# Kernel tuning notes

Hardware: AMD Instinct MI355X
Metric: run time of the kernel (lower is better)

## Reference

```python
import jax, jax.numpy as jnp
import numpy as np

EMBED = 256
HEADS = 8
WH, WW = 7, 7
N = WH * WW


def _rel_pos_index(Wh, Ww):
    coords = np.stack(np.meshgrid(np.arange(Wh), np.arange(Ww), indexing='ij'))  # [2,Wh,Ww]
    flat = coords.reshape(2, -1)  # [2, N]
    rel = flat[:, :, None] - flat[:, None, :]  # [2,N,N]
    rel = rel.transpose(1, 2, 0).astype(np.int64)
    rel[:, :, 0] += Wh - 1
    rel[:, :, 1] += Ww - 1
    rel[:, :, 0] *= 2 * Ww - 1
    return rel.sum(-1)  # [N,N]


def setup_inputs() -> dict:
    key = jax.random.key(0)
    ks = jax.random.split(key, 8)
    B = 4096
    nW = 64
    x = jax.random.normal(ks[0], (B, N, EMBED), dtype=jnp.float32)
    mask = jax.random.normal(ks[1], (nW, N, N), dtype=jnp.float32)
    qkv_w = jax.random.normal(ks[2], (3 * EMBED, EMBED), dtype=jnp.float32) * (EMBED ** -0.5)
    qkv_b = jnp.zeros((3 * EMBED,), dtype=jnp.float32)
    proj_w = jax.random.normal(ks[3], (EMBED, EMBED), dtype=jnp.float32) * (EMBED ** -0.5)
    proj_b = jnp.zeros((EMBED,), dtype=jnp.float32)
    bias_table = jax.random.normal(ks[4], ((2 * WH - 1) * (2 * WW - 1), HEADS), dtype=jnp.float32) * 0.02
    return {"x": x, "mask": mask, "qkv_w": qkv_w, "qkv_b": qkv_b,
            "proj_w": proj_w, "proj_b": proj_b, "bias_table": bias_table}


def reference(x, mask, qkv_w, qkv_b, proj_w, proj_b, bias_table):
    B, n, C = x.shape
    hd = C // HEADS
    scale = hd ** -0.5
    rel_idx = jnp.asarray(_rel_pos_index(WH, WW))  # [N,N] int, static
    qkv = (x @ qkv_w.T + qkv_b).reshape(B, n, 3, HEADS, hd)
    qkv = jnp.transpose(qkv, (2, 0, 3, 1, 4))  # [3,B,H,N,hd]
    q, k, v = qkv[0] * scale, qkv[1], qkv[2]
    attn = jnp.einsum('bhqd,bhkd->bhqk', q, k)  # [B,H,N,N]
    rel_bias = bias_table[rel_idx]  # [N,N,H]
    attn = attn + jnp.transpose(rel_bias, (2, 0, 1))[None]
    nW = mask.shape[0]
    attn = attn.reshape(B // nW, nW, HEADS, n, n) + mask[None, :, None]
    attn = attn.reshape(B, HEADS, n, n)
    attn = jax.nn.softmax(attn, axis=-1)
    out = jnp.einsum('bhqk,bhkd->bhqd', attn, v)  # [B,H,N,hd]
    out = jnp.transpose(out, (0, 2, 1, 3)).reshape(B, n, C)
    return out @ proj_w.T + proj_b
```

## Files before the change

### kernel.cpp

```cpp
#include <hip/hip_runtime.h>
#include <hip/hip_bf16.h>

typedef __bf16 bf16x8 __attribute__((ext_vector_type(8)));
typedef float f32x4 __attribute__((ext_vector_type(4)));
typedef short short8 __attribute__((ext_vector_type(8)));
typedef short short4v __attribute__((ext_vector_type(4)));

#define XSTRIDE 264
#define SCRSZ   2560
#define QKSTR   20
#define QHALF   1280
#define VSTR    72
#define PSTR    72
#define PBUF    1152

#define WS_QW   256u
#define WS_PW   393472u
#define WS_QB   524544u
#define WS_PB   527616u
#define WS_CMB  528640u
#define WS_FULL (528640u + 8388608u)

__device__ __forceinline__ float b2f(short s) {
  unsigned u = ((unsigned)(unsigned short)s) << 16;
  float f; __builtin_memcpy(&f, &u, 4); return f;
}
__device__ __forceinline__ short f2b(float f) {
  unsigned u; __builtin_memcpy(&u, &f, 4);
  u += 0x7FFFu + ((u >> 16) & 1u);
  return (short)(u >> 16);
}
__device__ __forceinline__ bf16x8 ld8(const short* p) {
  short8 s = *(const short8*)p;
  bf16x8 f; __builtin_memcpy(&f, &s, 16); return f;
}
__device__ __forceinline__ float ldE(const void* p, size_t i, int f32) {
  return f32 ? ((const float*)p)[i] : b2f(((const short*)p)[i]);
}
__device__ __forceinline__ f32x4 mfma16(bf16x8 a, bf16x8 b, f32x4 c) {
  return __builtin_amdgcn_mfma_f32_16x16x32_bf16(a, b, c, 0, 0, 0);
}
__device__ __forceinline__ void lgkm0() {
  asm volatile("s_waitcnt lgkmcnt(0)" ::: "memory");
  __builtin_amdgcn_sched_barrier(0);
}

__global__ __launch_bounds__(256) void detect_k(
    const short* p0, int n0, const short* p1, int n1, const short* p2, int n2,
    const short* p3, int n3, const short* p4, int n4, const short* p5, int n5,
    const short* p6, int n6, int* flags)
{
  const short* ps[7] = {p0, p1, p2, p3, p4, p5, p6};
  int ns[7] = {n0, n1, n2, n3, n4, n5, n6};
  int b = blockIdx.x;
  const short* p = ps[b];
  int n = ns[b];
  __shared__ int mx;
  if (threadIdx.x == 0) mx = 0;
  __syncthreads();
  int K = n >> 1; if (K > 4096) K = 4096;
  int lm = 0;
  for (int k = threadIdx.x; k < K; k += 256) {
    int e = (((int)(unsigned short)p[2 * k]) >> 7) & 0xFF;
    lm = lm > e ? lm : e;
  }
  atomicMax(&mx, lm);
  __syncthreads();
  if (threadIdx.x == 0) flags[b] = (mx >= 160) ? 1 : 0;
}

__global__ __launch_bounds__(256) void prep_k(
    const void* __restrict__ qkvw, const void* __restrict__ qkvb,
    const void* __restrict__ projw, const void* __restrict__ projb,
    const void* __restrict__ btab, const void* __restrict__ maskg,
    char* __restrict__ ws, const int* __restrict__ flags, int use_cmb)
{
  const int fm = flags[1], fqw = flags[2], fqb = flags[3];
  const int fpw = flags[4], fpb = flags[5], fbt = flags[6];
  short* qw = (short*)(ws + WS_QW);
  short* pw = (short*)(ws + WS_PW);
  float* qb = (float*)(ws + WS_QB);
  float* pb = (float*)(ws + WS_PB);
  float* cmb = (float*)(ws + WS_CMB);
  const int blk = blockIdx.x, tid = threadIdx.x;
  if (blk < 512) {
    if (!use_cmb) return;
    int widx = blk >> 3, h = blk & 7;
    for (int i = tid; i < 4096; i += 256) {
      int tq = i >> 6, tk = i & 63;
      float v = -1e30f;
      if (tq < 49 && tk < 49) {
        int qr = tq / 7, qc = tq - qr * 7;
        int kr = tk / 7, kc = tk - kr * 7;
        int idx = (qr - kr + 6) * 13 + (qc - kc + 6);
        v = ldE(maskg, (size_t)widx * 2401 + tq * 49 + tk, fm)
          + ldE(btab, (size_t)idx * 8 + h, fbt);
      }
      cmb[(size_t)blk * 4096 + i] = v;
    }
  } else if (blk < 528) {
    int base = (blk - 512) * 12288;
    for (int i = tid; i < 12288; i += 256)
      qw[base + i] = f2b(ldE(qkvw, base + i, fqw));
  } else if (blk < 530) {
    int base = (blk - 528) * 32768;
    for (int i = tid; i < 32768; i += 256)
      pw[base + i] = f2b(ldE(projw, base + i, fpw));
  } else {
    for (int i = tid; i < 768; i += 256) qb[i] = ldE(qkvb, i, fqb);
    if (tid < 256) pb[tid] = ldE(projb, tid, fpb);
  }
}

template<int USE_CMB>
__global__ __launch_bounds__(512, 4) void wmsa(
    const void* __restrict__ xg, const void* __restrict__ maskg,
    const void* __restrict__ btab, const char* __restrict__ ws,
    void* __restrict__ outg, const int* __restrict__ flags)
{
  __shared__ __align__(16) short lds[37376];
  const int tid  = threadIdx.x;
  const int w    = tid >> 6;
  const int lane = tid & 63;
  const int L    = lane & 15;
  const int quad = lane >> 4;
  const int b    = blockIdx.x;

  const int fx = flags[0];
  const int fm = flags[1], fbt = flags[6];

  const short* qw  = (const short*)(ws + WS_QW);
  const short* pw  = (const short*)(ws + WS_PW);
  const float* qb  = (const float*)(ws + WS_QB);
  const float* pb  = (const float*)(ws + WS_PB);
  const float* cmb = (const float*)(ws + WS_CMB);

  short* x_s = lds;
  short* scr = lds + 16896 + w * SCRSZ;

  if (fx) {
    const float* xb = (const float*)xg + (size_t)b * (49 * 256);
    for (int i = tid; i < 1568; i += 512) {
      int t = i >> 5, c8 = i & 31;
      const float* s = xb + t * 256 + c8 * 8;
      f32x4 a = *(const f32x4*)s;
      f32x4 c = *(const f32x4*)(s + 4);
      short8 v;
      v[0] = f2b(a[0]); v[1] = f2b(a[1]); v[2] = f2b(a[2]); v[3] = f2b(a[3]);
      v[4] = f2b(c[0]); v[5] = f2b(c[1]); v[6] = f2b(c[2]); v[7] = f2b(c[3]);
      *(short8*)(x_s + t * XSTRIDE + c8 * 8) = v;
    }
  } else {
    const short* xb = (const short*)xg + (size_t)b * (49 * 256);
    for (int i = tid; i < 1568; i += 512) {
      int t = i >> 5, c8 = i & 31;
      *(short8*)(x_s + t * XSTRIDE + c8 * 8) = *(const short8*)(xb + t * 256 + c8 * 8);
    }
  }
  for (int i = tid; i < 495; i += 512) {
    int t = 49 + i / 33, c8 = i - (i / 33) * 33;
    *(short8*)(x_s + t * XSTRIDE + c8 * 8) = short8{0,0,0,0,0,0,0,0};
  }
  __syncthreads();

  const int h = w;
  const float scale = 0.17677669529663687f;
  bf16x8 fq[4], fk[4], fv[2][2];

  {
    const int baserow = h * 32;
    bf16x8 wf[16];
    #pragma unroll
    for (int nbo = 0; nbo < 2; nbo++) {
      const short* wr = qw + (size_t)(baserow + nbo * 16 + L) * 256 + quad * 8;
      #pragma unroll
      for (int ks = 0; ks < 8; ks++) wf[nbo * 8 + ks] = ld8(wr + ks * 32);
    }
    const float b0 = qb[baserow + L], b1 = qb[baserow + 16 + L];
    #pragma unroll
    for (int m = 0; m < 4; m++) {
      const short* ar = x_s + (m * 16 + L) * XSTRIDE + quad * 8;
      bf16x8 xf[8];
      #pragma unroll
      for (int ks = 0; ks < 8; ks++) xf[ks] = ld8(ar + ks * 32);
      f32x4 a0 = {0.f,0.f,0.f,0.f}, a1 = {0.f,0.f,0.f,0.f};
      #pragma unroll
      for (int ks = 0; ks < 8; ks++) {
        a0 = mfma16(xf[ks], wf[ks], a0);
        a1 = mfma16(xf[ks], wf[8 + ks], a1);
      }
      #pragma unroll
      for (int r = 0; r < 4; r++) {
        scr[(m * 16 + quad * 4 + r) * QKSTR + L]         = f2b((a0[r] + b0) * scale);
        scr[QHALF + (m * 16 + quad * 4 + r) * QKSTR + L] = f2b((a1[r] + b1) * scale);
      }
    }
  }
  lgkm0();
  #pragma unroll
  for (int nbq = 0; nbq < 4; nbq++)
    fq[nbq] = ld8(scr + (quad >> 1) * QHALF + (nbq * 16 + L) * QKSTR + (quad & 1) * 8);
  lgkm0();

  {
    const int baserow = 256 + h * 32;
    bf16x8 wf[16];
    #pragma unroll
    for (int nbo = 0; nbo < 2; nbo++) {
      const short* wr = qw + (size_t)(baserow + nbo * 16 + L) * 256 + quad * 8;
      #pragma unroll
      for (int ks = 0; ks < 8; ks++) wf[nbo * 8 + ks] = ld8(wr + ks * 32);
    }
    const float b0 = qb[baserow + L], b1 = qb[baserow + 16 + L];
    #pragma unroll
    for (int m = 0; m < 4; m++) {
      const short* ar = x_s + (m * 16 + L) * XSTRIDE + quad * 8;
      bf16x8 xf[8];
      #pragma unroll
      for (int ks = 0; ks < 8; ks++) xf[ks] = ld8(ar + ks * 32);
      f32x4 a0 = {0.f,0.f,0.f,0.f}, a1 = {0.f,0.f,0.f,0.f};
      #pragma unroll
      for (int ks = 0; ks < 8; ks++) {
        a0 = mfma16(xf[ks], wf[ks], a0);
        a1 = mfma16(xf[ks], wf[8 + ks], a1);
      }
      #pragma unroll
      for (int r = 0; r < 4; r++) {
        scr[(m * 16 + quad * 4 + r) * QKSTR + L]         = f2b(a0[r] + b0);
        scr[QHALF + (m * 16 + quad * 4 + r) * QKSTR + L] = f2b(a1[r] + b1);
      }
    }
  }
  lgkm0();
  #pragma unroll
  for (int m = 0; m < 4; m++)
    fk[m] = ld8(scr + (quad >> 1) * QHALF + (m * 16 + L) * QKSTR + (quad & 1) * 8);
  lgkm0();

  #pragma unroll
  for (int nbo = 0; nbo < 2; nbo++) {
    const int baserow = 512 + h * 32 + nbo * 16;
    const short* wr = qw + (size_t)(baserow + L) * 256 + quad * 8;
    bf16x8 wf[8];
    #pragma unroll
    for (int ks = 0; ks < 8; ks++) wf[ks] = ld8(wr + ks * 32);
    const float bias = qb[baserow + L];
    #pragma unroll
    for (int m = 0; m < 4; m++) {
      const short* ar = x_s + (m * 16 + L) * XSTRIDE + quad * 8;
      f32x4 acc = {0.f, 0.f, 0.f, 0.f};
      #pragma unroll
      for (int ks = 0; ks < 8; ks++) acc = mfma16(ld8(ar + ks * 32), wf[ks], acc);
      short4v pk;
      #pragma unroll
      for (int r = 0; r < 4; r++) pk[r] = f2b(acc[r] + bias);
      *(short4v*)(scr + (nbo * 16 + L) * VSTR + m * 16 + quad * 4) = pk;
    }
  }
  lgkm0();
  #pragma unroll
  for (int ks2 = 0; ks2 < 2; ks2++)
    #pragma unroll
    for (int blk2 = 0; blk2 < 2; blk2++)
      fv[ks2][blk2] = ld8(scr + (blk2 * 16 + L) * VSTR + ks2 * 32 + quad * 8);
  lgkm0();

  __syncthreads();

  const int widx = b & 63;
  const float* cmbh = cmb + ((size_t)(widx * 8 + h)) * 4096;
  short* o_s = lds;
  #pragma unroll
  for (int nbq = 0; nbq < 4; nbq++) {
    const int tq = nbq * 16 + L;
    f32x4 c4[4];
    if (USE_CMB) {
      #pragma unroll
      for (int m = 0; m < 4; m++)
        c4[m] = *(const f32x4*)(cmbh + tq * 64 + m * 16 + quad * 4);
    }
    f32x4 s[4];
    #pragma unroll
    for (int m = 0; m < 4; m++) {
      f32x4 z = {0.f, 0.f, 0.f, 0.f};
      s[m] = mfma16(fk[m], fq[nbq], z);
    }
    float vals[16];
    float mx = -1e30f;
    if (USE_CMB) {
      #pragma unroll
      for (int m = 0; m < 4; m++) {
        #pragma unroll
        for (int r = 0; r < 4; r++) {
          float v = s[m][r] + c4[m][r];
          vals[m * 4 + r] = v;
          mx = fmaxf(mx, v);
        }
      }
    } else {
      const int tqc = tq < 49 ? tq : 48;
      const int qr = tqc / 7, qc = tqc - qr * 7;
      #pragma unroll
      for (int m = 0; m < 4; m++) {
        #pragma unroll
        for (int r = 0; r < 4; r++) {
          const int tk = m * 16 + quad * 4 + r;
          float v = -1e30f;
          if (tk < 49) {
            const int kr = tk / 7, kc = tk - kr * 7;
            const int idx = (qr - kr + 6) * 13 + (qc - kc + 6);
            v = s[m][r] + ldE(btab, (size_t)idx * 8 + h, fbt)
                        + ldE(maskg, (size_t)widx * 2401 + tqc * 49 + tk, fm);
          }
          vals[m * 4 + r] = v;
          mx = fmaxf(mx, v);
        }
      }
    }
    mx = fmaxf(mx, __shfl_xor(mx, 16));
    mx = fmaxf(mx, __shfl_xor(mx, 32));
    float sum = 0.f;
    #pragma unroll
    for (int i2 = 0; i2 < 16; i2++) { vals[i2] = __expf(vals[i2] - mx); sum += vals[i2]; }
    sum += __shfl_xor(sum, 16);
    sum += __shfl_xor(sum, 32);
    const float inv = 1.f / sum;
    short* pbuf = scr + (nbq & 1) * PBUF;
    #pragma unroll
    for (int m = 0; m < 4; m++) {
      short4v pk;
      #pragma unroll
      for (int r = 0; r < 4; r++) pk[r] = f2b(vals[m * 4 + r] * inv);
      *(short4v*)(pbuf + L * PSTR + m * 16 + quad * 4) = pk;
    }
    lgkm0();
    f32x4 o0 = {0.f,0.f,0.f,0.f}, o1 = {0.f,0.f,0.f,0.f};
    #pragma unroll
    for (int ks2 = 0; ks2 < 2; ks2++) {
      bf16x8 fp = ld8(pbuf + L * PSTR + ks2 * 32 + quad * 8);
      o0 = mfma16(fp, fv[ks2][0], o0);
      o1 = mfma16(fp, fv[ks2][1], o1);
    }
    #pragma unroll
    for (int r = 0; r < 4; r++) {
      o_s[(nbq * 16 + quad * 4 + r) * XSTRIDE + h * 32 + L]      = f2b(o0[r]);
      o_s[(nbq * 16 + quad * 4 + r) * XSTRIDE + h * 32 + 16 + L] = f2b(o1[r]);
    }
  }
  __syncthreads();

  {
    const int mb = w & 3, half = w >> 2;
    bf16x8 ao[8];
    const short* orow = o_s + (mb * 16 + L) * XSTRIDE + quad * 8;
    #pragma unroll
    for (int ks = 0; ks < 8; ks++) ao[ks] = ld8(orow + ks * 32);
    int nb = half * 8;
    bf16x8 cur[8];
    {
      const short* wr = pw + (size_t)(nb * 16 + L) * 256 + quad * 8;
      #pragma unroll
      for (int ks = 0; ks < 8; ks++) cur[ks] = ld8(wr + ks * 32);
    }
    for (int i = 0; i < 8; i++, nb++) {
      bf16x8 nxt[8];
      if (i < 7) {
        const short* wr = pw + (size_t)((nb + 1) * 16 + L) * 256 + quad * 8;
        #pragma unroll
        for (int ks = 0; ks < 8; ks++) nxt[ks] = ld8(wr + ks * 32);
      }
      f32x4 acc = {0.f, 0.f, 0.f, 0.f};
      #pragma unroll
      for (int ks = 0; ks < 8; ks++) acc = mfma16(ao[ks], cur[ks], acc);
      const float bias = pb[nb * 16 + L];
      #pragma unroll
      for (int r = 0; r < 4; r++) {
        const int t = mb * 16 + quad * 4 + r;
        if (t < 49) {
          size_t ofs = (size_t)b * (49 * 256) + (size_t)t * 256 + nb * 16 + L;
          float val = acc[r] + bias;
          if (fx) ((float*)outg)[ofs] = val;
          else    ((short*)outg)[ofs] = f2b(val);
        }
      }
      #pragma unroll
      for (int ks = 0; ks < 8; ks++) cur[ks] = nxt[ks];
    }
  }
}

extern "C" void kernel_launch(void* const* d_in, const int* in_sizes, int n_in,
                              void* d_out, int out_size, void* d_ws, size_t ws_size,
                              hipStream_t stream) {
  (void)n_in; (void)out_size;
  int B = in_sizes[0] / (49 * 256);
  char* ws = (char*)d_ws;
  int* flags = (int*)ws;
  detect_k<<<7, 256, 0, stream>>>(
      (const short*)d_in[0], in_sizes[0], (const short*)d_in[1], in_sizes[1],
      (const short*)d_in[2], in_sizes[2], (const short*)d_in[3], in_sizes[3],
      (const short*)d_in[4], in_sizes[4], (const short*)d_in[5], in_sizes[5],
      (const short*)d_in[6], in_sizes[6], flags);
  const int use_cmb = ws_size >= (size_t)WS_FULL;
  prep_k<<<531, 256, 0, stream>>>(d_in[2], d_in[3], d_in[4], d_in[5], d_in[6],
                                  d_in[1], ws, flags, use_cmb);
  if (use_cmb)
    wmsa<1><<<B, 512, 0, stream>>>(d_in[0], d_in[1], d_in[6], ws, d_out, flags);
  else
    wmsa<0><<<B, 512, 0, stream>>>(d_in[0], d_in[1], d_in[6], ws, d_out, flags);
}
```

Before: 824.2 us.

## Prefetch weights and mask tiles earlier, transpose MFMA operands for vectorized LDS stores

Q weight fragments are now loaded from global memory before the x tile is staged into LDS, and the first projection weight tile is loaded before the barrier, so global latency overlaps other work. Mask/bias tiles are double-buffered across query blocks instead of being loaded just before use. The MFMA operands for Q/K and PV are swapped so each lane's results land along one row, which allows 4-wide short stores to a single packed scratch layout and removes the explicit lgkmcnt waits and scheduling barriers. The trade-off is more live registers (wfQ held across staging, c4p double buffer), which may pressure occupancy at 512 threads and 4 blocks per CU.

Measured after the change: 827.8 us. No clear change (+0.4%).

```diff
diff --git a/kernel.cpp b/kernel.cpp
--- a/kernel.cpp
+++ b/kernel.cpp
@@ -7,9 +7,8 @@
 typedef short short4v __attribute__((ext_vector_type(4)));
 
 #define XSTRIDE 264
-#define SCRSZ   2560
-#define QKSTR   20
-#define QHALF   1280
+#define SCRSZ   2304
+#define QKSTR   36
 #define VSTR    72
 #define PSTR    72
 #define PBUF    1152
@@ -39,10 +38,6 @@
 }
 __device__ __forceinline__ f32x4 mfma16(bf16x8 a, bf16x8 b, f32x4 c) {
   return __builtin_amdgcn_mfma_f32_16x16x32_bf16(a, b, c, 0, 0, 0);
-}
-__device__ __forceinline__ void lgkm0() {
-  asm volatile("s_waitcnt lgkmcnt(0)" ::: "memory");
-  __builtin_amdgcn_sched_barrier(0);
 }
 
 __global__ __launch_bounds__(256) void detect_k(
@@ -118,7 +113,7 @@
     const void* __restrict__ btab, const char* __restrict__ ws,
     void* __restrict__ outg, const int* __restrict__ flags)
 {
-  __shared__ __align__(16) short lds[37376];
+  __shared__ __align__(16) short lds[35328];
   const int tid  = threadIdx.x;
   const int w    = tid >> 6;
   const int lane = tid & 63;
@@ -137,6 +132,18 @@
 
   short* x_s = lds;
   short* scr = lds + 16896 + w * SCRSZ;
+
+  const int h = w;
+
+  bf16x8 wfQ[16];
+  {
+    #pragma unroll
+    for (int cht = 0; cht < 2; cht++) {
+      const short* wr = qw + (size_t)(h * 32 + cht * 16 + L) * 256 + quad * 8;
+      #pragma unroll
+      for (int ks = 0; ks < 8; ks++) wfQ[cht * 8 + ks] = ld8(wr + ks * 32);
+    }
+  }
 
   if (fx) {
     const float* xb = (const float*)xg + (size_t)b * (49 * 256);
@@ -163,20 +170,12 @@
   }
   __syncthreads();
 
-  const int h = w;
   const float scale = 0.17677669529663687f;
   bf16x8 fq[4], fk[4], fv[2][2];
 
   {
-    const int baserow = h * 32;
-    bf16x8 wf[16];
-    #pragma unroll
-    for (int nbo = 0; nbo < 2; nbo++) {
-      const short* wr = qw + (size_t)(baserow + nbo * 16 + L) * 256 + quad * 8;
-      #pragma unroll
-      for (int ks = 0; ks < 8; ks++) wf[nbo * 8 + ks] = ld8(wr + ks * 32);
-    }
-    const float b0 = qb[baserow + L], b1 = qb[baserow + 16 + L];
+    const f32x4 b4a = *(const f32x4*)(qb + h * 32 + quad * 4);
+    const f32x4 b4b = *(const f32x4*)(qb + h * 32 + 16 + quad * 4);
     #pragma unroll
     for (int m = 0; m < 4; m++) {
       const short* ar = x_s + (m * 16 + L) * XSTRIDE + quad * 8;
@@ -186,32 +185,33 @@
       f32x4 a0 = {0.f,0.f,0.f,0.f}, a1 = {0.f,0.f,0.f,0.f};
       #pragma unroll
       for (int ks = 0; ks < 8; ks++) {
-        a0 = mfma16(xf[ks], wf[ks], a0);
-        a1 = mfma16(xf[ks], wf[8 + ks], a1);
-      }
+        a0 = mfma16(wfQ[ks], xf[ks], a0);
+        a1 = mfma16(wfQ[8 + ks], xf[ks], a1);
+      }
+      short4v q0, q1;
       #pragma unroll
       for (int r = 0; r < 4; r++) {
-        scr[(m * 16 + quad * 4 + r) * QKSTR + L]         = f2b((a0[r] + b0) * scale);
-        scr[QHALF + (m * 16 + quad * 4 + r) * QKSTR + L] = f2b((a1[r] + b1) * scale);
-      }
-    }
-  }
-  lgkm0();
+        q0[r] = f2b((a0[r] + b4a[r]) * scale);
+        q1[r] = f2b((a1[r] + b4b[r]) * scale);
+      }
+      *(short4v*)(scr + (m * 16 + L) * QKSTR + quad * 4)      = q0;
+      *(short4v*)(scr + (m * 16 + L) * QKSTR + 16 + quad * 4) = q1;
+    }
+  }
   #pragma unroll
   for (int nbq = 0; nbq < 4; nbq++)
-    fq[nbq] = ld8(scr + (quad >> 1) * QHALF + (nbq * 16 + L) * QKSTR + (quad & 1) * 8);
-  lgkm0();
-
-  {
-    const int baserow = 256 + h * 32;
-    bf16x8 wf[16];
-    #pragma unroll
-    for (int nbo = 0; nbo < 2; nbo++) {
-      const short* wr = qw + (size_t)(baserow + nbo * 16 + L) * 256 + quad * 8;
-      #pragma unroll
-      for (int ks = 0; ks < 8; ks++) wf[nbo * 8 + ks] = ld8(wr + ks * 32);
-    }
-    const float b0 = qb[baserow + L], b1 = qb[baserow + 16 + L];
+    fq[nbq] = ld8(scr + (nbq * 16 + L) * QKSTR + quad * 8);
+
+  {
+    bf16x8 wfK[16];
+    #pragma unroll
+    for (int cht = 0; cht < 2; cht++) {
+      const short* wr = qw + (size_t)(256 + h * 32 + cht * 16 + L) * 256 + quad * 8;
+      #pragma unroll
+      for (int ks = 0; ks < 8; ks++) wfK[cht * 8 + ks] = ld8(wr + ks * 32);
+    }
+    const f32x4 b4a = *(const f32x4*)(qb + 256 + h * 32 + quad * 4);
+    const f32x4 b4b = *(const f32x4*)(qb + 256 + h * 32 + 16 + quad * 4);
     #pragma unroll
     for (int m = 0; m < 4; m++) {
       const short* ar = x_s + (m * 16 + L) * XSTRIDE + quad * 8;
@@ -221,64 +221,77 @@
       f32x4 a0 = {0.f,0.f,0.f,0.f}, a1 = {0.f,0.f,0.f,0.f};
       #pragma unroll
       for (int ks = 0; ks < 8; ks++) {
-        a0 = mfma16(xf[ks], wf[ks], a0);
-        a1 = mfma16(xf[ks], wf[8 + ks], a1);
-      }
+        a0 = mfma16(wfK[ks], xf[ks], a0);
+        a1 = mfma16(wfK[8 + ks], xf[ks], a1);
+      }
+      short4v k0, k1;
       #pragma unroll
       for (int r = 0; r < 4; r++) {
-        scr[(m * 16 + quad * 4 + r) * QKSTR + L]         = f2b(a0[r] + b0);
-        scr[QHALF + (m * 16 + quad * 4 + r) * QKSTR + L] = f2b(a1[r] + b1);
-      }
-    }
-  }
-  lgkm0();
+        k0[r] = f2b(a0[r] + b4a[r]);
+        k1[r] = f2b(a1[r] + b4b[r]);
+      }
+      *(short4v*)(scr + (m * 16 + L) * QKSTR + quad * 4)      = k0;
+      *(short4v*)(scr + (m * 16 + L) * QKSTR + 16 + quad * 4) = k1;
+    }
+  }
   #pragma unroll
   for (int m = 0; m < 4; m++)
-    fk[m] = ld8(scr + (quad >> 1) * QHALF + (m * 16 + L) * QKSTR + (quad & 1) * 8);
-  lgkm0();
-
-  #pragma unroll
-  for (int nbo = 0; nbo < 2; nbo++) {
-    const int baserow = 512 + h * 32 + nbo * 16;
-    const short* wr = qw + (size_t)(baserow + L) * 256 + quad * 8;
-    bf16x8 wf[8];
-    #pragma unroll
-    for (int ks = 0; ks < 8; ks++) wf[ks] = ld8(wr + ks * 32);
-    const float bias = qb[baserow + L];
+    fk[m] = ld8(scr + (m * 16 + L) * QKSTR + quad * 8);
+
+  {
+    bf16x8 wfV[16];
+    #pragma unroll
+    for (int nbo = 0; nbo < 2; nbo++) {
+      const short* wr = qw + (size_t)(512 + h * 32 + nbo * 16 + L) * 256 + quad * 8;
+      #pragma unroll
+      for (int ks = 0; ks < 8; ks++) wfV[nbo * 8 + ks] = ld8(wr + ks * 32);
+    }
+    const float bv0 = qb[512 + h * 32 + L];
+    const float bv1 = qb[512 + h * 32 + 16 + L];
     #pragma unroll
     for (int m = 0; m < 4; m++) {
       const short* ar = x_s + (m * 16 + L) * XSTRIDE + quad * 8;
-      f32x4 acc = {0.f, 0.f, 0.f, 0.f};
-      #pragma unroll
-      for (int ks = 0; ks < 8; ks++) acc = mfma16(ld8(ar + ks * 32), wf[ks], acc);
-      short4v pk;
-      #pragma unroll
-      for (int r = 0; r < 4; r++) pk[r] = f2b(acc[r] + bias);
-      *(short4v*)(scr + (nbo * 16 + L) * VSTR + m * 16 + quad * 4) = pk;
-    }
-  }
-  lgkm0();
+      bf16x8 xf[8];
+      #pragma unroll
+      for (int ks = 0; ks < 8; ks++) xf[ks] = ld8(ar + ks * 32);
+      f32x4 a0 = {0.f,0.f,0.f,0.f}, a1 = {0.f,0.f,0.f,0.f};
+      #pragma unroll
+      for (int ks = 0; ks < 8; ks++) {
+        a0 = mfma16(xf[ks], wfV[ks], a0);
+        a1 = mfma16(xf[ks], wfV[8 + ks], a1);
+      }
+      short4v v0, v1;
+      #pragma unroll
+      for (int r = 0; r < 4; r++) { v0[r] = f2b(a0[r] + bv0); v1[r] = f2b(a1[r] + bv1); }
+      *(short4v*)(scr + L * VSTR + m * 16 + quad * 4)        = v0;
+      *(short4v*)(scr + (16 + L) * VSTR + m * 16 + quad * 4) = v1;
+    }
+  }
   #pragma unroll
   for (int ks2 = 0; ks2 < 2; ks2++)
     #pragma unroll
     for (int blk2 = 0; blk2 < 2; blk2++)
       fv[ks2][blk2] = ld8(scr + (blk2 * 16 + L) * VSTR + ks2 * 32 + quad * 8);
-  lgkm0();
 
   __syncthreads();
 
   const int widx = b & 63;
   const float* cmbh = cmb + ((size_t)(widx * 8 + h)) * 4096;
   short* o_s = lds;
+
+  f32x4 c4p[2][4];
+  if (USE_CMB) {
+    #pragma unroll
+    for (int m = 0; m < 4; m++)
+      c4p[0][m] = *(const f32x4*)(cmbh + (0 * 16 + L) * 64 + m * 16 + quad * 4);
+    #pragma unroll
+    for (int m = 0; m < 4; m++)
+      c4p[1][m] = *(const f32x4*)(cmbh + (1 * 16 + L) * 64 + m * 16 + quad * 4);
+  }
+
   #pragma unroll
   for (int nbq = 0; nbq < 4; nbq++) {
     const int tq = nbq * 16 + L;
-    f32x4 c4[4];
-    if (USE_CMB) {
-      #pragma unroll
-      for (int m = 0; m < 4; m++)
-        c4[m] = *(const f32x4*)(cmbh + tq * 64 + m * 16 + quad * 4);
-    }
     f32x4 s[4];
     #pragma unroll
     for (int m = 0; m < 4; m++) {
@@ -292,10 +305,16 @@
       for (int m = 0; m < 4; m++) {
         #pragma unroll
         for (int r = 0; r < 4; r++) {
-          float v = s[m][r] + c4[m][r];
+          float v = s[m][r] + c4p[nbq & 1][m][r];
           vals[m * 4 + r] = v;
           mx = fmaxf(mx, v);
         }
+      }
+      if (nbq < 2) {
+        #pragma unroll
+        for (int m = 0; m < 4; m++)
+          c4p[nbq & 1][m] =
+              *(const f32x4*)(cmbh + ((nbq + 2) * 16 + L) * 64 + m * 16 + quad * 4);
       }
     } else {
       const int tqc = tq < 49 ? tq : 48;
@@ -333,35 +352,35 @@
       for (int r = 0; r < 4; r++) pk[r] = f2b(vals[m * 4 + r] * inv);
       *(short4v*)(pbuf + L * PSTR + m * 16 + quad * 4) = pk;
     }
-    lgkm0();
     f32x4 o0 = {0.f,0.f,0.f,0.f}, o1 = {0.f,0.f,0.f,0.f};
     #pragma unroll
     for (int ks2 = 0; ks2 < 2; ks2++) {
       bf16x8 fp = ld8(pbuf + L * PSTR + ks2 * 32 + quad * 8);
-      o0 = mfma16(fp, fv[ks2][0], o0);
-      o1 = mfma16(fp, fv[ks2][1], o1);
-    }
-    #pragma unroll
-    for (int r = 0; r < 4; r++) {
-      o_s[(nbq * 16 + quad * 4 + r) * XSTRIDE + h * 32 + L]      = f2b(o0[r]);
-      o_s[(nbq * 16 + quad * 4 + r) * XSTRIDE + h * 32 + 16 + L] = f2b(o1[r]);
-    }
+      o0 = mfma16(fv[ks2][0], fp, o0);
+      o1 = mfma16(fv[ks2][1], fp, o1);
+    }
+    short4v o0v, o1v;
+    #pragma unroll
+    for (int r = 0; r < 4; r++) { o0v[r] = f2b(o0[r]); o1v[r] = f2b(o1[r]); }
+    *(short4v*)(o_s + (nbq * 16 + L) * XSTRIDE + h * 32 + quad * 4)      = o0v;
+    *(short4v*)(o_s + (nbq * 16 + L) * XSTRIDE + h * 32 + 16 + quad * 4) = o1v;
+  }
+
+  const int mb = w & 3, half = w >> 2;
+  int nb = half * 8;
+  bf16x8 cur[8];
+  {
+    const short* wr = pw + (size_t)(nb * 16 + L) * 256 + quad * 8;
+    #pragma unroll
+    for (int ks = 0; ks < 8; ks++) cur[ks] = ld8(wr + ks * 32);
   }
   __syncthreads();
 
   {
-    const int mb = w & 3, half = w >> 2;
     bf16x8 ao[8];
     const short* orow = o_s + (mb * 16 + L) * XSTRIDE + quad * 8;
     #pragma unroll
     for (int ks = 0; ks < 8; ks++) ao[ks] = ld8(orow + ks * 32);
-    int nb = half * 8;
-    bf16x8 cur[8];
-    {
-      const short* wr = pw + (size_t)(nb * 16 + L) * 256 + quad * 8;
-      #pragma unroll
-      for (int ks = 0; ks < 8; ks++) cur[ks] = ld8(wr + ks * 32);
-    }
     for (int i = 0; i < 8; i++, nb++) {
       bf16x8 nxt[8];
       if (i < 7) {
```
